# Kernel tuning notes

Measured on AMD Instinct MI355X. Metric: run time of the kernel, lower is better.

## Reference

```python
import jax, jax.numpy as jnp
import numpy as np

N = 4194304  # number of 3D points (surfels)
H, W = 1024, 1280


def setup_inputs() -> dict:
    key = jax.random.key(0)
    k1, k2, k3 = jax.random.split(key, 3)
    # camera-frame points: x,y in [-0.5, 0.5], z (depth) in [0.5, 2.5]
    xy = jax.random.uniform(k1, (N, 2), dtype=jnp.float32, minval=-0.5, maxval=0.5)
    z = jax.random.uniform(k2, (N, 1), dtype=jnp.float32, minval=0.5, maxval=2.5)
    points = jnp.concatenate([xy, z], axis=-1)
    colors = jax.random.uniform(k3, (N, 3), dtype=jnp.float32)
    fx = fy = 1000.0
    K = jnp.array([[fx, 0.0, W / 2.0], [0.0, fy, H / 2.0], [0.0, 0.0, 1.0]],
                  dtype=jnp.float32)
    return {"points": points, "colors": colors, "K": K, "height": H, "width": W}


def reference(points, colors, K, height, width):
    # pcd2depth: pinhole projection with rounding
    fx, fy, cx, cy = K[0, 0], K[1, 1], K[0, 2], K[1, 2]
    z = points[:, 2]
    u = jnp.round(fx * points[:, 0] / z + cx).astype(jnp.int32)
    v = jnp.round(fy * points[:, 1] / z + cy).astype(jnp.int32)
    valid = (z > 0) & (u >= 0) & (u < width) & (v >= 0) & (v < height)
    n = points.shape[0]
    npix = height * width
    # sentinel pixel npix for invalid points
    flat = jnp.where(valid, v * width + u, npix)
    # far-to-near overwrite after depth_sort=True)
    order = jnp.argsort(jnp.where(valid, z, jnp.inf))  # ascending depth
    flat_sorted = flat[order]
    ranks = jnp.arange(n, dtype=jnp.int32)
    # per-pixel min rank (rank = position in depth-ascending order)
    win = jnp.full(npix + 1, n, dtype=jnp.int32).at[flat_sorted].min(ranks)
    win = win[:npix]
    has_point = win < n
    winner = order[jnp.minimum(win, n - 1)]  # point index per pixel
    img = jnp.where(has_point[:, None], colors[winner].astype(jnp.float32), 0.0)
    return img.reshape(height, width, 3)
```

## Files before the change

### kernel.cpp

```cpp
#include <hip/hip_runtime.h>
#include <stdint.h>

#define NPTS    4194304
#define IMG_H   1024
#define IMG_W   1280
#define NPIX    (IMG_H * IMG_W)

#define TW      40
#define TH      32
#define TILES_X (IMG_W / TW)
#define TILES_Y (IMG_H / TH)
#define NBINS   (TILES_X * TILES_Y)
#define TPIX    (TW * TH)

#define NBLK    768
#define TPB     256
#define TPB_R   256
#define SEGS_PER_T (NBLK / TPB_R)
#if (NBLK % TPB_R) != 0
#error "NBLK must be a multiple of TPB_R"
#endif

#define CHUNK_Q ((NPTS / 4 + NBLK - 1) / NBLK)
#define CHUNK_P (CHUNK_Q * 4)
#define SSTRIDE CHUNK_P
#define QPT     ((CHUNK_Q + TPB - 1) / TPB)
#define BPT     (NBINS / TPB)

static const unsigned long long KEY_SENTINEL = ~0ULL;
#define KEY47_MASK ((1ULL << 47) - 1)


struct Perm { unsigned short p[NBINS]; };
constexpr Perm make_perm() {
    unsigned short rank[NBINS] = {};
    float score[NBINS] = {};
    for (int i = 0; i < NBINS; ++i) {
        int tx = i % TILES_X, ty = i / TILES_X;
        float du = ((float)tx + 0.5f) * (float)TW - 640.0f;
        float dv = ((float)ty + 0.5f) * (float)TH - 512.0f;
        du /= 640.0f; dv /= 512.0f;
        score[i] = du * du + dv * dv;
        rank[i] = (unsigned short)i;
    }
    for (int i = 1; i < NBINS; ++i) {
        unsigned short key = rank[i];
        float ks = score[key];
        int j = i - 1;
        while (j >= 0 && score[rank[j]] > ks) { rank[j + 1] = rank[j]; --j; }
        rank[j + 1] = key;
    }
    Perm P{};
    for (int i = 0; i < NBINS; ++i) {
        int r = i / 256, k = i % 256;
        int src = (r & 1) ? (r * 256 + (255 - k)) : (r * 256 + k);
        P.p[i] = rank[src];
    }
    return P;
}
__device__ __constant__ Perm c_perm = make_perm();

__device__ __forceinline__ bool project(float x, float y, float z,
                                        float fx, float fy, float cx, float cy,
                                        int& u, int& v) {
    float uf = rintf(fx * x / z + cx);
    float vf = rintf(fy * y / z + cy);
    bool valid = (z > 0.0f) &&
                 (uf >= 0.0f) && (uf < (float)IMG_W) &&
                 (vf >= 0.0f) && (vf < (float)IMG_H);
    u = (int)uf;
    v = (int)vf;
    return valid;
}

__device__ __forceinline__ unsigned int zc_of(float z) {
    unsigned int zb = __float_as_uint(z);
    unsigned int zc = zb - 0x3F000000u;
    if ((int)zc < 0) zc = 0;
    if (zc > 0x1FFFFFFu) zc = 0x1FFFFFFu;
    return zc;
}

__global__ __launch_bounds__(TPB, 3) void pass_bin(
        const float4* __restrict__ pts4, const float* __restrict__ Kmat,
        unsigned int* __restrict__ cnt_off ,
        unsigned long long* __restrict__ grec ,
        int n_quads, int qchunk) {
    __shared__ unsigned long long srec[CHUNK_P];
    __shared__ unsigned int hist[NBINS];
    __shared__ unsigned int cur[NBINS];
    __shared__ unsigned int tsum[TPB];

    int t   = threadIdx.x;
    int blk = blockIdx.x;
#pragma unroll
    for (int i = t; i < NBINS; i += TPB) hist[i] = 0;
    __syncthreads();

    float fx = Kmat[0], cx = Kmat[2];
    float fy = Kmat[4], cy = Kmat[5];

    int q0 = blk * qchunk;
    int q1 = min(n_quads, q0 + qchunk);

    unsigned long long keep[QPT * 4];

#pragma unroll
    for (int qi = 0; qi < QPT; ++qi) {
        int q = q0 + t + qi * TPB;
        bool inb = (q < q1);
        float4 a = {}, b = {}, c = {};
        if (inb) {
            a = pts4[3 * q + 0];
            b = pts4[3 * q + 1];
            c = pts4[3 * q + 2];
        }
        float px[4] = {a.x, a.w, b.z, c.y};
        float py[4] = {a.y, b.x, b.w, c.z};
        float pz[4] = {a.z, b.y, c.x, c.w};
#pragma unroll
        for (int k = 0; k < 4; ++k) {
            unsigned long long kv = ~0ULL;
            int u, v;
            if (inb && project(px[k], py[k], pz[k], fx, fy, cx, cy, u, v)) {
                int tx  = u / TW;
                int bin = (v >> 5) * TILES_X + tx;
                unsigned int pos = (unsigned int)((v & 31) * TW + (u - tx * TW));
                atomicAdd(&hist[bin], 1u);
                kv = ((unsigned long long)bin << 36) |
                     ((unsigned long long)pos << 25) |
                     (unsigned long long)zc_of(pz[k]);
            }
            keep[qi * 4 + k] = kv;
        }
    }
    __syncthreads();

    unsigned int hv[BPT];
    {
        unsigned int s = 0;
#pragma unroll
        for (int j = 0; j < BPT; ++j) { hv[j] = hist[BPT * t + j]; s += hv[j]; }
        tsum[t] = s;
    }
    __syncthreads();
    for (int off = 1; off < TPB; off <<= 1) {
        unsigned int x = (t >= off) ? tsum[t - off] : 0u;
        __syncthreads();
        tsum[t] += x;
        __syncthreads();
    }
    {
        unsigned int run = (t > 0) ? tsum[t - 1] : 0u;
#pragma unroll
        for (int j = 0; j < BPT; ++j) {
            cur[BPT * t + j] = run;
            run += hv[j];
        }
    }
    __syncthreads();

#pragma unroll
    for (int i = t; i < NBINS; i += TPB)
        cnt_off[(size_t)i * NBLK + blk] = (hist[i] << 16) | cur[i];
    __syncthreads();

#pragma unroll
    for (int qi = 0; qi < QPT; ++qi) {
        int q = q0 + t + qi * TPB;
        unsigned int i0 = 4u * (unsigned int)q;
#pragma unroll
        for (int k = 0; k < 4; ++k) {
            unsigned long long kv = keep[qi * 4 + k];
            if (kv != ~0ULL) {
                int bin          = (int)(kv >> 36);
                unsigned int pos = (unsigned int)((kv >> 25) & 0x7FFu);
                unsigned int zc  = (unsigned int)(kv & 0x1FFFFFFu);
                unsigned int slot = atomicAdd(&cur[bin], 1u);
                srec[slot] = ((unsigned long long)pos << 47) |
                             ((unsigned long long)zc << 22) |
                             (unsigned long long)(i0 + (unsigned int)k);
            }
        }
    }
    __syncthreads();

    unsigned int nrec = cur[NBINS - 1];
    unsigned long long* my = grec + (size_t)blk * SSTRIDE;
    for (unsigned int i = t; i < nrec; i += TPB) my[i] = srec[i];
}

__global__ __launch_bounds__(TPB_R) void pass_render(
        const unsigned long long* __restrict__ grec,
        const unsigned int* __restrict__ cnt_off ,
        const float* __restrict__ colors,
        float* __restrict__ out, int npts) {
    __shared__ unsigned long long key[TPIX];

    int t = threadIdx.x;
    int b = c_perm.p[blockIdx.x];

#pragma unroll
    for (int i = t; i < TPIX; i += TPB_R) key[i] = KEY_SENTINEL;

    unsigned int w[SEGS_PER_T];
#pragma unroll
    for (int s = 0; s < SEGS_PER_T; ++s)
        w[s] = cnt_off[(size_t)b * NBLK + (t + s * TPB_R)];
    __syncthreads();

#pragma unroll
    for (int s = 0; s < SEGS_PER_T; ++s) {
        unsigned int cnt = w[s] >> 16;
        unsigned int off = w[s] & 0xFFFFu;
        const unsigned long long* seg =
            grec + (size_t)(t + s * TPB_R) * SSTRIDE + off;
        if ((off & 1u) && cnt) {
            unsigned long long rec = seg[0];
            atomicMin(&key[(unsigned int)(rec >> 47)], rec & KEY47_MASK);
            ++seg; --cnt;
        }
        const ulonglong2* seg2 = (const ulonglong2*)seg;
        unsigned int np = cnt >> 1;
        unsigned int p = 0;
        for (; p + 2 <= np; p += 2) {
            ulonglong2 a  = seg2[p];
            ulonglong2 b2 = seg2[p + 1];
            atomicMin(&key[(unsigned int)(a.x  >> 47)], a.x  & KEY47_MASK);
            atomicMin(&key[(unsigned int)(a.y  >> 47)], a.y  & KEY47_MASK);
            atomicMin(&key[(unsigned int)(b2.x >> 47)], b2.x & KEY47_MASK);
            atomicMin(&key[(unsigned int)(b2.y >> 47)], b2.y & KEY47_MASK);
        }
        if (p < np) {
            ulonglong2 a = seg2[p];
            atomicMin(&key[(unsigned int)(a.x >> 47)], a.x & KEY47_MASK);
            atomicMin(&key[(unsigned int)(a.y >> 47)], a.y & KEY47_MASK);
        }
        if (cnt & 1u) {
            unsigned long long rec = seg[cnt - 1];
            atomicMin(&key[(unsigned int)(rec >> 47)], rec & KEY47_MASK);
        }
    }
    __syncthreads();

    int tx = b % TILES_X, ty = b / TILES_X;
#pragma unroll
    for (int i = t; i < TPIX; i += TPB_R) {
        int row = i / TW, col = i - row * TW;
        unsigned long long kk = key[i];
        float r = 0.0f, g = 0.0f, bl = 0.0f;
        if (kk != KEY_SENTINEL) {
            unsigned int idx = (unsigned int)(kk & 0x3FFFFFu);
            if (idx + 1u < (unsigned int)npts) {
                float4 c4 = *(const float4*)(colors + 3u * idx);
                r = c4.x; g = c4.y; bl = c4.z;
            } else {
                r  = colors[3u * idx + 0];
                g  = colors[3u * idx + 1];
                bl = colors[3u * idx + 2];
            }
        }
        size_t gp = (size_t)(ty * TH + row) * IMG_W + (size_t)(tx * TW + col);
        out[3 * gp + 0] = r;
        out[3 * gp + 1] = g;
        out[3 * gp + 2] = bl;
    }
}

__global__ void init_keys_vec(ulonglong2* __restrict__ keys, int n_vec2) {
    int i = blockIdx.x * blockDim.x + threadIdx.x;
    if (i < n_vec2) keys[i] = ulonglong2{~0ULL, ~0ULL};
}

__global__ void scatter_points_pretest(const float4* __restrict__ pts4,
                                       const float* __restrict__ Kmat,
                                       unsigned long long* __restrict__ keys,
                                       int n_quads) {
    int t = blockIdx.x * blockDim.x + threadIdx.x;
    if (t >= n_quads) return;
    float fx = Kmat[0], cx = Kmat[2];
    float fy = Kmat[4], cy = Kmat[5];
    float4 a = pts4[3 * t + 0];
    float4 b = pts4[3 * t + 1];
    float4 c = pts4[3 * t + 2];
    float px[4] = {a.x, a.w, b.z, c.y};
    float py[4] = {a.y, b.x, b.w, c.z};
    float pz[4] = {a.z, b.y, c.x, c.w};
    unsigned int i0 = 4u * (unsigned int)t;
#pragma unroll
    for (int k = 0; k < 4; ++k) {
        int u, v;
        if (!project(px[k], py[k], pz[k], fx, fy, cx, cy, u, v)) continue;
        int pix = v * IMG_W + u;
        unsigned long long key =
            ((unsigned long long)__float_as_uint(pz[k]) << 32) | (i0 + k);
        if (key < keys[pix]) atomicMin(&keys[pix], key);
    }
}

__global__ void resolve_pixels4(const unsigned long long* __restrict__ keys,
                                const float* __restrict__ colors,
                                float* __restrict__ out, int n_quads) {
    int t = blockIdx.x * blockDim.x + threadIdx.x;
    if (t >= n_quads) return;
    int base = 4 * t;
    ulonglong2 k01 = *(const ulonglong2*)(keys + base);
    ulonglong2 k23 = *(const ulonglong2*)(keys + base + 2);
    unsigned long long kk[4] = {k01.x, k01.y, k23.x, k23.y};
    float c[12];
#pragma unroll
    for (int j = 0; j < 4; ++j) {
        float r = 0.0f, g = 0.0f, b = 0.0f;
        if (kk[j] != KEY_SENTINEL) {
            unsigned int idx = (unsigned int)(kk[j] & 0xFFFFFFFFu);
            r = colors[3 * idx + 0];
            g = colors[3 * idx + 1];
            b = colors[3 * idx + 2];
        }
        c[3 * j + 0] = r; c[3 * j + 1] = g; c[3 * j + 2] = b;
    }
    float4* o = (float4*)(out + 3 * (size_t)base);
    o[0] = float4{c[0], c[1], c[2],  c[3]};
    o[1] = float4{c[4], c[5], c[6],  c[7]};
    o[2] = float4{c[8], c[9], c[10], c[11]};
}

extern "C" void kernel_launch(void* const* d_in, const int* in_sizes, int n_in,
                              void* d_out, int out_size, void* d_ws, size_t ws_size,
                              hipStream_t stream) {
    const float4* pts4  = (const float4*)d_in[0];
    const float* colors = (const float*)d_in[1];
    const float* Kmat   = (const float*)d_in[2];
    float* out = (float*)d_out;

    int n       = in_sizes[0] / 3;
    int n_quads = n / 4;
    int qchunk  = (n_quads + NBLK - 1) / NBLK;

    char* ws = (char*)d_ws;
    size_t off = 0;
    auto alloc = [&](size_t bytes) {
        char* p = ws + off;
        off += (bytes + 63) & ~(size_t)63;
        return p;
    };
    unsigned int*       cnt_off = (unsigned int*)alloc((size_t)NBLK * NBINS * 4);
    unsigned long long* grec =
        (unsigned long long*)alloc((size_t)NBLK * SSTRIDE * 8);

    if (qchunk <= CHUNK_Q && ws_size >= off) {
        pass_bin<<<NBLK, TPB, 0, stream>>>(pts4, Kmat, cnt_off, grec,
                                           n_quads, qchunk);
        pass_render<<<NBINS, TPB_R, 0, stream>>>(grec, cnt_off, colors, out, n);
    } else {
        unsigned long long* keys = (unsigned long long*)d_ws;
        const int B = 256;
        int n_vec2 = NPIX / 2;
        init_keys_vec<<<(n_vec2 + B - 1) / B, B, 0, stream>>>(
            (ulonglong2*)keys, n_vec2);
        scatter_points_pretest<<<(n_quads + B - 1) / B, B, 0, stream>>>(
            pts4, Kmat, keys, n_quads);
        int npix_quads = NPIX / 4;
        resolve_pixels4<<<(npix_quads + B - 1) / B, B, 0, stream>>>(
            keys, colors, out, npix_quads);
    }
}
```

Before: 167.7 us.

## Raise binning block count and write count table row-major with separate transpose

Increases the number of binning blocks from 768 to 1280, which shrinks each block's point chunk and shared staging so four blocks can be resident per CU. The per-block count/offset table is now written contiguously per block (coalesced) and then transposed by a new tiled shared-memory kernel into the bin-major layout the render pass reads. This removes strided global stores in the binning pass at the cost of an extra kernel launch, an extra workspace buffer, and more segments per render thread to walk.

```diff
diff --git a/kernel.cpp b/kernel.cpp
--- a/kernel.cpp
+++ b/kernel.cpp
@@ -13,7 +13,7 @@
 #define NBINS   (TILES_X * TILES_Y)
 #define TPIX    (TW * TH)
 
-#define NBLK    768
+#define NBLK    1280
 #define TPB     256
 #define TPB_R   256
 #define SEGS_PER_T (NBLK / TPB_R)
@@ -81,7 +81,7 @@
     return zc;
 }
 
-__global__ __launch_bounds__(TPB, 3) void pass_bin(
+__global__ __launch_bounds__(TPB, 4) void pass_bin(
         const float4* __restrict__ pts4, const float* __restrict__ Kmat,
         unsigned int* __restrict__ cnt_off ,
         unsigned long long* __restrict__ grec ,
@@ -162,7 +162,7 @@
 
 #pragma unroll
     for (int i = t; i < NBINS; i += TPB)
-        cnt_off[(size_t)i * NBLK + blk] = (hist[i] << 16) | cur[i];
+        cnt_off[(size_t)blk * NBINS + i] = (hist[i] << 16) | cur[i];
     __syncthreads();
 
 #pragma unroll
@@ -190,9 +190,30 @@
     for (unsigned int i = t; i < nrec; i += TPB) my[i] = srec[i];
 }
 
+__global__ __launch_bounds__(256) void transpose_table(
+        const unsigned int* __restrict__ in ,
+        unsigned int* __restrict__ outT     ) {
+    __shared__ unsigned int tile[32][33];
+    int t  = threadIdx.x;
+    int tx = t & 31, ty = t >> 5;
+    int bx = blockIdx.x % (NBINS / 32);
+    int by = blockIdx.x / (NBINS / 32);
+#pragma unroll
+    for (int i = 0; i < 4; ++i) {
+        int r = by * 32 + ty + i * 8;
+        tile[ty + i * 8][tx] = in[(size_t)r * NBINS + (bx * 32 + tx)];
+    }
+    __syncthreads();
+#pragma unroll
+    for (int i = 0; i < 4; ++i) {
+        int r = bx * 32 + ty + i * 8;
+        outT[(size_t)r * NBLK + (by * 32 + tx)] = tile[tx][ty + i * 8];
+    }
+}
+
 __global__ __launch_bounds__(TPB_R) void pass_render(
         const unsigned long long* __restrict__ grec,
-        const unsigned int* __restrict__ cnt_off ,
+        const unsigned int* __restrict__ cnt_offT ,
         const float* __restrict__ colors,
         float* __restrict__ out, int npts) {
     __shared__ unsigned long long key[TPIX];
@@ -206,7 +227,7 @@
     unsigned int w[SEGS_PER_T];
 #pragma unroll
     for (int s = 0; s < SEGS_PER_T; ++s)
-        w[s] = cnt_off[(size_t)b * NBLK + (t + s * TPB_R)];
+        w[s] = cnt_offT[(size_t)b * NBLK + (t + s * TPB_R)];
     __syncthreads();
 
 #pragma unroll
@@ -344,14 +365,17 @@
         off += (bytes + 63) & ~(size_t)63;
         return p;
     };
-    unsigned int*       cnt_off = (unsigned int*)alloc((size_t)NBLK * NBINS * 4);
+    unsigned int*       cnt_off  = (unsigned int*)alloc((size_t)NBLK * NBINS * 4);
+    unsigned int*       cnt_offT = (unsigned int*)alloc((size_t)NBLK * NBINS * 4);
     unsigned long long* grec =
         (unsigned long long*)alloc((size_t)NBLK * SSTRIDE * 8);
 
     if (qchunk <= CHUNK_Q && ws_size >= off) {
         pass_bin<<<NBLK, TPB, 0, stream>>>(pts4, Kmat, cnt_off, grec,
                                            n_quads, qchunk);
-        pass_render<<<NBINS, TPB_R, 0, stream>>>(grec, cnt_off, colors, out, n);
+        transpose_table<<<(NBINS / 32) * (NBLK / 32), 256, 0, stream>>>(
+            cnt_off, cnt_offT);
+        pass_render<<<NBINS, TPB_R, 0, stream>>>(grec, cnt_offT, colors, out, n);
     } else {
         unsigned long long* keys = (unsigned long long*)d_ws;
         const int B = 256;
```

Measured after the change: 169.1 us. Within noise of the previous version (+0.8%).
